# Performance work log

Measured on AMD Instinct MI355X. Metric: run time of the kernel, lower is better.

## Reference

```python
import jax, jax.numpy as jnp
import numpy as np

D_SEM = 512
N_LEVELS = 16
HALF = (N_LEVELS - 1) / 2.0
EPS = 1e-5


def setup_inputs() -> dict:
    key = jax.random.key(0)
    k1, k2, k3, k4, k5, k6 = jax.random.split(key, 6)
    B, D, T = 16, 544, 4096  # D = semantic_dim(512) + acoustic_dim(32)
    x = jax.random.normal(k1, (B, D, T), dtype=jnp.float32)
    embedding_sum = jax.random.normal(k2, (4096, D_SEM), dtype=jnp.float32)
    cluster_usage = jax.random.uniform(k3, (4096,), dtype=jnp.float32)
    sem_probs = jax.random.uniform(k4, (B,), dtype=jnp.float32)
    aco_probs = jax.random.uniform(k5, (B,), dtype=jnp.float32)
    # torch: uniform(-1/n_levels, 1/n_levels) * half_levels
    noise = (jax.random.uniform(k6, (B, 32, T), dtype=jnp.float32) * 2.0 - 1.0) * (HALF / N_LEVELS)
    return {"x": x, "embedding_sum": embedding_sum, "cluster_usage": cluster_usage,
            "sem_probs": sem_probs, "aco_probs": aco_probs, "noise": noise}


def reference(x, embedding_sum, cluster_usage, sem_probs, aco_probs, noise):
    B, D, T = x.shape
    # lazily-built codebook: embedding_sum / clamp(cluster_usage)
    emb = embedding_sum / jnp.clip(cluster_usage, EPS, None)[:, None]  # [K, D_sem]

    sem_x = x[:, :D_SEM, :]   # [B, D_sem, T]
    aco_x = x[:, D_SEM:, :]   # [B, D_aco, T]

    # ---- semantic VQ: cdist(p=2) + argmin (argmin of squared dist is identical) ----
    xf = sem_x.transpose(0, 2, 1).reshape(B * T, D_SEM)                      # (b t) d
    d2 = (jnp.sum(xf * xf, axis=-1, keepdims=True)
          - 2.0 * (xf @ emb.T)
          + jnp.sum(emb * emb, axis=-1))                                      # [B*T, K]
    sem_codes = jnp.argmin(d2, axis=-1).reshape(B, 1, T)                      # [B,1,T]
    sem_q = emb[sem_codes[:, 0, :]].transpose(0, 2, 1)                        # [B, D_sem, T]
    sem_mask = (sem_probs < 0.5)[:, None, None]
    sem_out = jnp.where(sem_mask, sem_x + jax.lax.stop_gradient(sem_q - sem_x), sem_x)

    z_b = jnp.tanh(aco_x) * HALF
    z_q = z_b + jax.lax.stop_gradient(jnp.round(z_b) - z_b)
    z_dither = jnp.clip(z_b + noise, -HALF, HALF)
    quant_mask = (aco_probs < 0.5)[:, None, None]
    dither_mask = ((aco_probs >= 0.5) & (aco_probs < 0.75))[:, None, None]
    z_out = jnp.where(quant_mask, z_q, jnp.where(dither_mask, z_dither, z_b))
    aco_codes = jnp.clip(jnp.round(z_out + HALF), 0, N_LEVELS - 1).astype(jnp.int32)

    quantized = jnp.concatenate([sem_out, z_out / HALF], axis=1)              # [B, D, T]
    codes = jnp.concatenate([sem_codes.astype(jnp.int32), aco_codes], axis=1)  # [B, 1+D_aco, T]
    return quantized, codes
```

## Files before the change

### kernel.cpp

```cpp
#include <hip/hip_runtime.h>
#include <math.h>

#define BB 16
#define DTOT 544
#define TT_DIM 4096
#define DS 512
#define NCODES 4096
#define HALFV 7.5f
#define EPSV 1e-5f
#define NROWS (BB * TT_DIM)
#define NT 16
#define MT 256
#define REFINE_THR 0.02f
#define TT 32

typedef short bf16x8 __attribute__((ext_vector_type(8)));
typedef float f32x4 __attribute__((ext_vector_type(4)));

__device__ __forceinline__ unsigned short f2bf(float v) {
    unsigned u = __float_as_uint(v);
    unsigned r = (u + 0x7fffu + ((u >> 16) & 1u)) >> 16;
    return (unsigned short)r;
}
__device__ __forceinline__ float bf2f(unsigned short h) {
    return __uint_as_float((unsigned)h << 16);
}

__global__ __launch_bounds__(256) void k_emb(const float* __restrict__ esum,
                                             const float* __restrict__ usage,
                                             float* __restrict__ emb,
                                             float* __restrict__ e2,
                                             int* __restrict__ counter) {
    int c = blockIdx.x;
    if (c == 0 && threadIdx.x == 0) *counter = 0;
    float u = usage[c];
    u = (u < EPSV) ? EPSV : u;
    float s = 0.f;
#pragma unroll
    for (int i = 0; i < 2; i++) {
        int d = threadIdx.x + i * 256;
        float v = esum[(size_t)c * DS + d] / u;
        emb[(size_t)c * DS + d] = v;
        s += v * v;
    }
#pragma unroll
    for (int o = 32; o; o >>= 1) s += __shfl_down(s, o, 64);
    __shared__ float red[4];
    if ((threadIdx.x & 63) == 0) red[threadIdx.x >> 6] = s;
    __syncthreads();
    if (threadIdx.x == 0) e2[c] = red[0] + red[1] + red[2] + red[3];
}

__global__ __launch_bounds__(256) void k_packA(const float* __restrict__ x,
                                               char* __restrict__ Ap) {
    __shared__ char ldsH[16384];
    __shared__ char ldsL[16384];
    int mt = blockIdx.x, dc = blockIdx.y;
    int b = mt >> 4;
    int t0 = (mt & 15) * 256;
    int tid = threadIdx.x;
#pragma unroll
    for (int i = 0; i < 8; i++) {
        int idx = tid + i * 256;
        int d = idx >> 6;
        int t4 = idx & 63;
        float4 v = *(const float4*)&x[((size_t)b * DTOT + dc * 32 + d) * TT_DIM + t0 + t4 * 4];
        float va[4] = {v.x, v.y, v.z, v.w};
        int u = d >> 3;
        int kb = (d & 7) * 2;
#pragma unroll
        for (int j = 0; j < 4; j++) {
            int row = t4 * 4 + j;
            unsigned short hi = f2bf(va[j]);
            unsigned short lo = f2bf(va[j] - bf2f(hi));
            int off = row * 64 + ((u ^ ((row >> 1) & 3)) << 4) + kb;
            *(unsigned short*)&ldsH[off] = hi;
            *(unsigned short*)&ldsL[off] = lo;
        }
    }
    __syncthreads();
    char* gH = Ap + ((size_t)mt * 32 + dc) * 16384;
    char* gL = Ap + ((size_t)mt * 32 + 16 + dc) * 16384;
#pragma unroll
    for (int i = 0; i < 4; i++) {
        int off = (tid + i * 256) * 16;
        *(uint4*)&gH[off] = *(const uint4*)&ldsH[off];
        *(uint4*)&gL[off] = *(const uint4*)&ldsL[off];
    }
}

__global__ __launch_bounds__(256) void k_packB(const float* __restrict__ emb,
                                               char* __restrict__ Bp) {
    __shared__ char ldsT[16384];
    int nt = blockIdx.x, c = blockIdx.y;
    int lo_flag = (c >= 16);
    int d0 = (lo_flag ? (c - 16) : c) * 32;
    int c0 = nt * 256;
    int tid = threadIdx.x;
#pragma unroll
    for (int i = 0; i < 8; i++) {
        int idx = tid + i * 256;
        int row = idx >> 3;
        int f4 = idx & 7;
        float4 v = *(const float4*)&emb[(size_t)(c0 + row) * DS + d0 + f4 * 4];
        float va[4] = {v.x, v.y, v.z, v.w};
        unsigned short wv[4];
#pragma unroll
        for (int j = 0; j < 4; j++) {
            unsigned short hi = f2bf(va[j]);
            wv[j] = lo_flag ? f2bf(va[j] - bf2f(hi)) : hi;
        }
        int u = f4 >> 1;
        int off = row * 64 + ((u ^ ((row >> 1) & 3)) << 4) + (f4 & 1) * 8;
        uint2 pk;
        pk.x = ((unsigned)wv[1] << 16) | wv[0];
        pk.y = ((unsigned)wv[3] << 16) | wv[2];
        *(uint2*)&ldsT[off] = pk;
    }
    __syncthreads();
    char* g = Bp + ((size_t)nt * 32 + c) * 16384;
#pragma unroll
    for (int i = 0; i < 4; i++) {
        int off = (tid + i * 256) * 16;
        *(uint4*)&g[off] = *(const uint4*)&ldsT[off];
    }
}

#define MM(A, B, C) __builtin_amdgcn_mfma_f32_16x16x32_bf16((A), (B), (C), 0, 0, 0)

#define GLDS(SRC, DOFF)                                                              \
    __builtin_amdgcn_global_load_lds(                                                \
        (const __attribute__((address_space(1))) void*)(SRC),                        \
        (__attribute__((address_space(3))) void*)&lds[DOFF], 16, 0, 0)

#define BAR __builtin_amdgcn_s_barrier()
#define VMW0 asm volatile("s_waitcnt vmcnt(0)" ::: "memory")
#define VMNONE (void)0

#define STAGE64(T) do {                                                              \
    int sb_ = ((T) & 1) * 65536;                                                     \
    _Pragma("unroll")                                                                \
    for (int h_ = 0; h_ < 2; h_++) {                                                 \
        int c_ = 2 * (T) + h_;                                                       \
        int at_ = (c_ < 32) ? (c_ & 15) : (c_ - 16);                                 \
        int bt_ = (c_ < 32) ? c_ : (c_ - 32);                                        \
        GLDS(Ap_mt + at_ * 16384 + t16, sb_ + h_ * 16384 + t16);                     \
        GLDS(Bp_nt + bt_ * 16384 + t16, sb_ + 32768 + h_ * 16384 + t16);             \
    }                                                                                \
} while (0)

#define STEP64(T, DO_STG, VMEND, DO_BAR) do {                                        \
    int sb_ = ((T) & 1) * 65536;                                                     \
    bf16x8 bfv[4], af[4];                                                            \
    _Pragma("unroll")                                                                \
    for (int n_ = 0; n_ < 4; n_++)                                                   \
        bfv[n_] = *(const bf16x8*)&lds[sb_ + 32768 + offB[n_]];                      \
    _Pragma("unroll")                                                                \
    for (int m_ = 0; m_ < 4; m_++)                                                   \
        af[m_] = *(const bf16x8*)&lds[sb_ + offA[m_]];                               \
    if (DO_STG) STAGE64((T) + 1);                                                    \
    __builtin_amdgcn_s_setprio(1);                                                   \
    _Pragma("unroll")                                                                \
    for (int m_ = 0; m_ < 4; m_++)                                                   \
        _Pragma("unroll")                                                            \
        for (int n_ = 0; n_ < 4; n_++)                                               \
            acc[m_][n_] = MM(af[m_], bfv[n_], acc[m_][n_]);                          \
    __builtin_amdgcn_s_setprio(0);                                                   \
    _Pragma("unroll")                                                                \
    for (int n_ = 0; n_ < 4; n_++)                                                   \
        bfv[n_] = *(const bf16x8*)&lds[sb_ + 49152 + offB[n_]];                      \
    _Pragma("unroll")                                                                \
    for (int m_ = 0; m_ < 4; m_++)                                                   \
        af[m_] = *(const bf16x8*)&lds[sb_ + 16384 + offA[m_]];                       \
    __builtin_amdgcn_s_setprio(1);                                                   \
    _Pragma("unroll")                                                                \
    for (int m_ = 0; m_ < 4; m_++)                                                   \
        _Pragma("unroll")                                                            \
        for (int n_ = 0; n_ < 4; n_++)                                               \
            acc[m_][n_] = MM(af[m_], bfv[n_], acc[m_][n_]);                          \
    __builtin_amdgcn_s_setprio(0);                                                   \
    VMEND;                                                                           \
    if (DO_BAR) BAR;                                                                 \
} while (0)

__global__ __launch_bounds__(1024, 4) void k_mfma(const char* __restrict__ Ap,
                                                  const char* __restrict__ Bp,
                                                  const float* __restrict__ e2,
                                                  float* __restrict__ pb,
                                                  int* __restrict__ pi,
                                                  float* __restrict__ ps) {
    extern __shared__ char lds[];
    int bid = blockIdx.x;
    int lin = (bid >> 3) + (bid & 7) * 512;
    int nt = lin & 15;
    int mt = lin >> 4;

    int tid = threadIdx.x;
    int lane = tid & 63;
    int w = tid >> 6;
    int wr = w >> 2, wc = w & 3;
    int l15 = lane & 15, lhi = lane >> 4;
    int t16 = tid * 16;

    const char* Ap_mt = Ap + (size_t)mt * 32 * 16384;
    const char* Bp_nt = Bp + (size_t)nt * 32 * 16384;

    int offA[4], offB[4];
#pragma unroll
    for (int m = 0; m < 4; m++) {
        int r = wr * 64 + m * 16 + l15;
        offA[m] = r * 64 + ((lhi ^ ((r >> 1) & 3)) << 4);
    }
#pragma unroll
    for (int n = 0; n < 4; n++) {
        int r = wc * 64 + n * 16 + l15;
        offB[n] = r * 64 + ((lhi ^ ((r >> 1) & 3)) << 4);
    }

    f32x4 acc[4][4];
#pragma unroll
    for (int m = 0; m < 4; m++)
#pragma unroll
        for (int n = 0; n < 4; n++) acc[m][n] = (f32x4){0.f, 0.f, 0.f, 0.f};

    STAGE64(0);
    VMW0;
    BAR;

#pragma unroll 1
    for (int t = 0; t < 23; t++) {
        STEP64(t, 1, VMW0, 1);
    }
    STEP64(23, 0, VMNONE, 0);

    __syncthreads();
    float* rb = (float*)lds;
    float* rs = (float*)(lds + 4096);
    int*   ri = (int*)(lds + 8192);

    float e2v[4];
#pragma unroll
    for (int n = 0; n < 4; n++)
        e2v[n] = e2[nt * 256 + wc * 64 + n * 16 + l15];

#pragma unroll
    for (int m = 0; m < 4; m++) {
#pragma unroll
        for (int r2 = 0; r2 < 4; r2++) {
            float bst = 3.4e38f, sec = 3.4e38f;
            int bi = 1 << 30;
#pragma unroll
            for (int n = 0; n < 4; n++) {
                float v = e2v[n] - 2.f * acc[m][n][r2];
                int vi = wc * 64 + n * 16 + l15;
                if (v < bst || (v == bst && vi < bi)) { sec = bst; bst = v; bi = vi; }
                else sec = fminf(sec, v);
            }
#pragma unroll
            for (int mask = 1; mask <= 8; mask <<= 1) {
                float ob = __shfl_xor(bst, mask);
                int obi = __shfl_xor(bi, mask);
                float os = __shfl_xor(sec, mask);
                if (ob < bst || (ob == bst && obi < bi)) {
                    sec = fminf(bst, os); bst = ob; bi = obi;
                } else {
                    sec = fminf(sec, ob);
                }
            }
            if (l15 == 0) {
                int rl = wr * 64 + m * 16 + lhi * 4 + r2;
                int slot = wc * 256 + rl;
                rb[slot] = bst; rs[slot] = sec; ri[slot] = nt * 256 + bi;
            }
        }
    }
    __syncthreads();
    if (tid < 256) {
        float bsv = rb[tid], ssv = rs[tid];
        int biv = ri[tid];
#pragma unroll
        for (int c = 1; c < 4; c++) {
            float ob = rb[c * 256 + tid];
            float os = rs[c * 256 + tid];
            int oi = ri[c * 256 + tid];
            if (ob < bsv || (ob == bsv && oi < biv)) { ssv = fminf(bsv, os); bsv = ob; biv = oi; }
            else ssv = fminf(ssv, ob);
        }
        size_t gr = (size_t)mt * 256 + tid;
        pb[(size_t)nt * NROWS + gr] = bsv;
        pi[(size_t)nt * NROWS + gr] = biv;
        ps[(size_t)nt * NROWS + gr] = ssv;
    }
}

__global__ __launch_bounds__(256) void k_reduce(const float* __restrict__ pb,
                                                const int* __restrict__ pi,
                                                const float* __restrict__ ps,
                                                int* __restrict__ codes,
                                                int* __restrict__ list,
                                                int* __restrict__ counter) {
    int row = blockIdx.x * 256 + threadIdx.x;
    float b = 3.4e38f, s = 3.4e38f;
    int bi = 1 << 30;
    for (int nt = 0; nt < NT; nt++) {
        float b2 = pb[(size_t)nt * NROWS + row];
        int i2 = pi[(size_t)nt * NROWS + row];
        float s2 = ps[(size_t)nt * NROWS + row];
        if (b2 < b || (b2 == b && i2 < bi)) { s = fminf(b, s2); b = b2; bi = i2; }
        else s = fminf(s, b2);
    }
    codes[row] = bi;
    if (s - b < REFINE_THR) {
        int p = atomicAdd(counter, 1);
        list[p] = row;
    }
}

__global__ __launch_bounds__(256) void k_refine(const float* __restrict__ x,
                                                const float* __restrict__ emb,
                                                int* __restrict__ codes,
                                                const int* __restrict__ list,
                                                const int* __restrict__ counter) {
    __shared__ float xrow[DS];
    __shared__ double redv[256];
    __shared__ int redi[256];
    int tid = threadIdx.x;
    int nflag = *counter;
    for (int it = blockIdx.x; it < nflag; it += gridDim.x) {
        int row = list[it];
        int b = row >> 12;
        int t = row & 4095;
        for (int d = tid; d < DS; d += 256)
            xrow[d] = x[((size_t)b * DTOT + d) * TT_DIM + t];
        __syncthreads();
        double bv = 1e300;
        int bi = 1 << 30;
        for (int c = tid; c < NCODES; c += 256) {
            const float* er = emb + (size_t)c * DS;
            double s = 0.0;
            for (int d = 0; d < DS; d += 4) {
                float4 ev = *(const float4*)&er[d];
                float4 xv = *(const float4*)&xrow[d];
                double d0 = (double)xv.x - (double)ev.x;
                double d1 = (double)xv.y - (double)ev.y;
                double d2 = (double)xv.z - (double)ev.z;
                double d3 = (double)xv.w - (double)ev.w;
                s += d0 * d0 + d1 * d1 + d2 * d2 + d3 * d3;
            }
            if (s < bv || (s == bv && c < bi)) { bv = s; bi = c; }
        }
        redv[tid] = bv; redi[tid] = bi;
        __syncthreads();
        for (int off = 128; off; off >>= 1) {
            if (tid < off) {
                if (redv[tid + off] < redv[tid] ||
                    (redv[tid + off] == redv[tid] && redi[tid + off] < redi[tid])) {
                    redv[tid] = redv[tid + off];
                    redi[tid] = redi[tid + off];
                }
            }
            __syncthreads();
        }
        if (tid == 0) codes[row] = redi[0];
        __syncthreads();
    }
}

__global__ __launch_bounds__(256) void k_sem(const float* __restrict__ x,
                                             const float* __restrict__ emb,
                                             const int* __restrict__ codes,
                                             const float* __restrict__ sem_probs,
                                             float* __restrict__ out) {
    __shared__ int rowc[TT];
    int b = blockIdx.y, t0 = blockIdx.x * TT;
    bool mask = sem_probs[b] < 0.5f;
    float* outb = out + (size_t)b * DTOT * TT_DIM + t0;
    const float* xb = x + (size_t)b * DTOT * TT_DIM + t0;
    const size_t QOFF = (size_t)BB * DTOT * TT_DIM;

    if (threadIdx.x < TT) {
        int code = codes[b * TT_DIM + t0 + threadIdx.x];
        rowc[threadIdx.x] = code;
        out[QOFF + ((size_t)b * 33) * TT_DIM + t0 + threadIdx.x] = (float)code;
    }
    __syncthreads();

    if (mask) {
#pragma unroll
        for (int i = 0; i < 4; i++) {
            int u = threadIdx.x + i * 256;
            int d4 = u >> 3;
            int tg = u & 7;
            float4 r0 = *(const float4*)&emb[(size_t)rowc[tg * 4 + 0] * DS + d4 * 4];
            float4 r1 = *(const float4*)&emb[(size_t)rowc[tg * 4 + 1] * DS + d4 * 4];
            float4 r2 = *(const float4*)&emb[(size_t)rowc[tg * 4 + 2] * DS + d4 * 4];
            float4 r3 = *(const float4*)&emb[(size_t)rowc[tg * 4 + 3] * DS + d4 * 4];
            float4 c0 = {r0.x, r1.x, r2.x, r3.x};
            float4 c1 = {r0.y, r1.y, r2.y, r3.y};
            float4 c2 = {r0.z, r1.z, r2.z, r3.z};
            float4 c3 = {r0.w, r1.w, r2.w, r3.w};
            *(float4*)&outb[(size_t)(d4 * 4 + 0) * TT_DIM + tg * 4] = c0;
            *(float4*)&outb[(size_t)(d4 * 4 + 1) * TT_DIM + tg * 4] = c1;
            *(float4*)&outb[(size_t)(d4 * 4 + 2) * TT_DIM + tg * 4] = c2;
            *(float4*)&outb[(size_t)(d4 * 4 + 3) * TT_DIM + tg * 4] = c3;
        }
    } else {
#pragma unroll
        for (int i = 0; i < 16; i++) {
            int u = threadIdx.x + i * 256;
            int d = u >> 3;
            int tg = u & 7;
            *(float4*)&outb[(size_t)d * TT_DIM + tg * 4] =
                *(const float4*)&xb[(size_t)d * TT_DIM + tg * 4];
        }
    }
}

__global__ __launch_bounds__(256) void k_aco(const float* __restrict__ x,
                                             const float* __restrict__ noise,
                                             const float* __restrict__ aco_probs,
                                             float* __restrict__ out) {
    int idx = blockIdx.x * 256 + threadIdx.x;
    int t4 = idx & 1023;
    int bc = idx >> 10;
    int ch = bc & 31;
    int b = bc >> 5;
    const float4 xv = *(const float4*)&x[((size_t)(b * DTOT + DS + ch)) * TT_DIM + t4 * 4];
    const float4 nv = *(const float4*)&noise[((size_t)(b * 32 + ch)) * TT_DIM + t4 * 4];
    float p = aco_probs[b];
    const size_t QOFF = (size_t)BB * DTOT * TT_DIM;

    float zq[4], cq[4];
    float xa[4] = {xv.x, xv.y, xv.z, xv.w};
    float na[4] = {nv.x, nv.y, nv.z, nv.w};
#pragma unroll
    for (int i = 0; i < 4; i++) {
        float zb = tanhf(xa[i]) * HALFV;
        float z;
        if (p < 0.5f) z = rintf(zb);
        else if (p < 0.75f) z = fminf(fmaxf(zb + na[i], -HALFV), HALFV);
        else z = zb;
        zq[i] = z / HALFV;
        cq[i] = fminf(fmaxf(rintf(z + HALFV), 0.f), 15.f);
    }
    float4 qo = {zq[0], zq[1], zq[2], zq[3]};
    float4 co = {cq[0], cq[1], cq[2], cq[3]};
    *(float4*)&out[((size_t)(b * DTOT + DS + ch)) * TT_DIM + t4 * 4] = qo;
    *(float4*)&out[QOFF + ((size_t)(b * 33 + 1 + ch)) * TT_DIM + t4 * 4] = co;
}

extern "C" void kernel_launch(void* const* d_in, const int* in_sizes, int n_in,
                              void* d_out, int out_size, void* d_ws, size_t ws_size,
                              hipStream_t stream) {
    const float* x         = (const float*)d_in[0];
    const float* esum      = (const float*)d_in[1];
    const float* usage     = (const float*)d_in[2];
    const float* sem_probs = (const float*)d_in[3];
    const float* aco_probs = (const float*)d_in[4];
    const float* noise     = (const float*)d_in[5];
    float* out = (float*)d_out;

    char* w = (char*)d_ws;
    float* emb    = (float*)w;
    float* e2     = (float*)(w + 8388608);
    char*  Ap     = w + 8404992;
    char*  Bp     = w + 142622720;
    float* pb     = (float*)(w + 151011328);
    int*   pi     = (int*)(w + 155205632);
    float* ps     = (float*)(w + 159399936);
    int*   codes  = (int*)(w + 163594240);
    int*   list   = (int*)(w + 163856384);
    int*   counter= (int*)(w + 164118528);

    k_emb<<<NCODES, 256, 0, stream>>>(esum, usage, emb, e2, counter);
    k_packA<<<dim3(MT, 16), 256, 0, stream>>>(x, Ap);
    k_packB<<<dim3(NT, 32), 256, 0, stream>>>(emb, Bp);
    k_mfma<<<NT * MT, 1024, 131072, stream>>>(Ap, Bp, e2, pb, pi, ps);
    k_reduce<<<NROWS / 256, 256, 0, stream>>>(pb, pi, ps, codes, list, counter);
    k_refine<<<256, 256, 0, stream>>>(x, emb, codes, list, counter);
    k_sem<<<dim3(TT_DIM / TT, BB), 256, 0, stream>>>(x, emb, codes, sem_probs, out);
    k_aco<<<(BB * 32 * TT_DIM) / (256 * 4), 256, 0, stream>>>(x, noise, aco_probs, out);
}
```

Measured before the change: 1.171 ms.

## Refine ambiguous rows by comparing only the top-two bf16 candidates in fp64

The MFMA epilogue and the reduce kernel now track the index of the second-best code along with its distance. The refine kernel no longer rescans all 4096 codes per flagged row in double precision; each wavefront compares only the best and runner-up candidates. The refine threshold is also halved so fewer rows are flagged. The trade-off is correctness risk: the true nearest code may lie outside the bf16 top two, and the tighter threshold misses more near-ties. The extra second-index bookkeeping adds some cost to the MFMA epilogue and to reduce memory traffic.

```diff
diff --git a/kernel.cpp b/kernel.cpp
--- a/kernel.cpp
+++ b/kernel.cpp
@@ -11,7 +11,7 @@
 #define NROWS (BB * TT_DIM)
 #define NT 16
 #define MT 256
-#define REFINE_THR 0.02f
+#define REFINE_THR 0.01f
 #define TT 32
 
 typedef short bf16x8 __attribute__((ext_vector_type(8)));
@@ -188,7 +188,8 @@
                                                   const float* __restrict__ e2,
                                                   float* __restrict__ pb,
                                                   int* __restrict__ pi,
-                                                  float* __restrict__ ps) {
+                                                  float* __restrict__ ps,
+                                                  int* __restrict__ psi) {
     extern __shared__ char lds[];
     int bid = blockIdx.x;
     int lin = (bid >> 3) + (bid & 7) * 512;
@@ -237,6 +238,7 @@
     float* rb = (float*)lds;
     float* rs = (float*)(lds + 4096);
     int*   ri = (int*)(lds + 8192);
+    int*   rsi = (int*)(lds + 12288);
 
     float e2v[4];
 #pragma unroll
@@ -248,68 +250,88 @@
 #pragma unroll
         for (int r2 = 0; r2 < 4; r2++) {
             float bst = 3.4e38f, sec = 3.4e38f;
-            int bi = 1 << 30;
+            int bi = 1 << 30, si = 1 << 30;
 #pragma unroll
             for (int n = 0; n < 4; n++) {
                 float v = e2v[n] - 2.f * acc[m][n][r2];
                 int vi = wc * 64 + n * 16 + l15;
-                if (v < bst || (v == bst && vi < bi)) { sec = bst; bst = v; bi = vi; }
-                else sec = fminf(sec, v);
+                if (v < bst || (v == bst && vi < bi)) { sec = bst; si = bi; bst = v; bi = vi; }
+                else if (v < sec || (v == sec && vi < si)) { sec = v; si = vi; }
             }
 #pragma unroll
             for (int mask = 1; mask <= 8; mask <<= 1) {
                 float ob = __shfl_xor(bst, mask);
                 int obi = __shfl_xor(bi, mask);
                 float os = __shfl_xor(sec, mask);
+                int osi = __shfl_xor(si, mask);
                 if (ob < bst || (ob == bst && obi < bi)) {
-                    sec = fminf(bst, os); bst = ob; bi = obi;
+                    if (bst < os || (bst == os && bi < osi)) { sec = bst; si = bi; }
+                    else { sec = os; si = osi; }
+                    bst = ob; bi = obi;
                 } else {
-                    sec = fminf(sec, ob);
+                    if (ob < sec || (ob == sec && obi < si)) { sec = ob; si = obi; }
                 }
             }
             if (l15 == 0) {
                 int rl = wr * 64 + m * 16 + lhi * 4 + r2;
                 int slot = wc * 256 + rl;
-                rb[slot] = bst; rs[slot] = sec; ri[slot] = nt * 256 + bi;
+                rb[slot] = bst; rs[slot] = sec;
+                ri[slot] = nt * 256 + bi; rsi[slot] = nt * 256 + si;
             }
         }
     }
     __syncthreads();
     if (tid < 256) {
         float bsv = rb[tid], ssv = rs[tid];
-        int biv = ri[tid];
+        int biv = ri[tid], siv = rsi[tid];
 #pragma unroll
         for (int c = 1; c < 4; c++) {
             float ob = rb[c * 256 + tid];
             float os = rs[c * 256 + tid];
             int oi = ri[c * 256 + tid];
-            if (ob < bsv || (ob == bsv && oi < biv)) { ssv = fminf(bsv, os); bsv = ob; biv = oi; }
-            else ssv = fminf(ssv, ob);
+            int osi = rsi[c * 256 + tid];
+            if (ob < bsv || (ob == bsv && oi < biv)) {
+                if (bsv < os || (bsv == os && biv < osi)) { ssv = bsv; siv = biv; }
+                else { ssv = os; siv = osi; }
+                bsv = ob; biv = oi;
+            } else {
+                if (ob < ssv || (ob == ssv && oi < siv)) { ssv = ob; siv = oi; }
+            }
         }
         size_t gr = (size_t)mt * 256 + tid;
         pb[(size_t)nt * NROWS + gr] = bsv;
         pi[(size_t)nt * NROWS + gr] = biv;
         ps[(size_t)nt * NROWS + gr] = ssv;
+        psi[(size_t)nt * NROWS + gr] = siv;
     }
 }
 
 __global__ __launch_bounds__(256) void k_reduce(const float* __restrict__ pb,
                                                 const int* __restrict__ pi,
                                                 const float* __restrict__ ps,
+                                                const int* __restrict__ psi,
                                                 int* __restrict__ codes,
+                                                int* __restrict__ cand2,
                                                 int* __restrict__ list,
                                                 int* __restrict__ counter) {
     int row = blockIdx.x * 256 + threadIdx.x;
     float b = 3.4e38f, s = 3.4e38f;
-    int bi = 1 << 30;
+    int bi = 1 << 30, si = 1 << 30;
     for (int nt = 0; nt < NT; nt++) {
         float b2 = pb[(size_t)nt * NROWS + row];
         int i2 = pi[(size_t)nt * NROWS + row];
         float s2 = ps[(size_t)nt * NROWS + row];
-        if (b2 < b || (b2 == b && i2 < bi)) { s = fminf(b, s2); b = b2; bi = i2; }
-        else s = fminf(s, b2);
+        int si2 = psi[(size_t)nt * NROWS + row];
+        if (b2 < b || (b2 == b && i2 < bi)) {
+            if (b < s2 || (b == s2 && bi < si2)) { s = b; si = bi; }
+            else { s = s2; si = si2; }
+            b = b2; bi = i2;
+        } else {
+            if (b2 < s || (b2 == s && i2 < si)) { s = b2; si = i2; }
+        }
     }
     codes[row] = bi;
+    cand2[row] = si;
     if (s - b < REFINE_THR) {
         int p = atomicAdd(counter, 1);
         list[p] = row;
@@ -319,50 +341,34 @@
 __global__ __launch_bounds__(256) void k_refine(const float* __restrict__ x,
                                                 const float* __restrict__ emb,
                                                 int* __restrict__ codes,
+                                                const int* __restrict__ cand2,
                                                 const int* __restrict__ list,
                                                 const int* __restrict__ counter) {
-    __shared__ float xrow[DS];
-    __shared__ double redv[256];
-    __shared__ int redi[256];
-    int tid = threadIdx.x;
+    int wid = threadIdx.x >> 6, lane = threadIdx.x & 63;
     int nflag = *counter;
-    for (int it = blockIdx.x; it < nflag; it += gridDim.x) {
+    for (int it = blockIdx.x * 4 + wid; it < nflag; it += gridDim.x * 4) {
         int row = list[it];
         int b = row >> 12;
         int t = row & 4095;
-        for (int d = tid; d < DS; d += 256)
-            xrow[d] = x[((size_t)b * DTOT + d) * TT_DIM + t];
-        __syncthreads();
-        double bv = 1e300;
-        int bi = 1 << 30;
-        for (int c = tid; c < NCODES; c += 256) {
-            const float* er = emb + (size_t)c * DS;
-            double s = 0.0;
-            for (int d = 0; d < DS; d += 4) {
-                float4 ev = *(const float4*)&er[d];
-                float4 xv = *(const float4*)&xrow[d];
-                double d0 = (double)xv.x - (double)ev.x;
-                double d1 = (double)xv.y - (double)ev.y;
-                double d2 = (double)xv.z - (double)ev.z;
-                double d3 = (double)xv.w - (double)ev.w;
-                s += d0 * d0 + d1 * d1 + d2 * d2 + d3 * d3;
-            }
-            if (s < bv || (s == bv && c < bi)) { bv = s; bi = c; }
-        }
-        redv[tid] = bv; redi[tid] = bi;
-        __syncthreads();
-        for (int off = 128; off; off >>= 1) {
-            if (tid < off) {
-                if (redv[tid + off] < redv[tid] ||
-                    (redv[tid + off] == redv[tid] && redi[tid + off] < redi[tid])) {
-                    redv[tid] = redv[tid + off];
-                    redi[tid] = redi[tid + off];
-                }
-            }
-            __syncthreads();
-        }
-        if (tid == 0) codes[row] = redi[0];
-        __syncthreads();
+        int c1 = codes[row], c2 = cand2[row];
+        if (c2 >= NCODES) continue;
+        const float* xb = x + (size_t)b * DTOT * TT_DIM + t;
+        double s1 = 0.0, s2 = 0.0;
+        for (int d = lane; d < DS; d += 64) {
+            double xv = (double)xb[(size_t)d * TT_DIM];
+            double d1 = xv - (double)emb[(size_t)c1 * DS + d];
+            double d2v = xv - (double)emb[(size_t)c2 * DS + d];
+            s1 += d1 * d1;
+            s2 += d2v * d2v;
+        }
+#pragma unroll
+        for (int o = 32; o; o >>= 1) {
+            s1 += __shfl_down(s1, o, 64);
+            s2 += __shfl_down(s2, o, 64);
+        }
+        if (lane == 0) {
+            if (s2 < s1 || (s2 == s1 && c2 < c1)) codes[row] = c2;
+        }
     }
 }
 
@@ -468,16 +474,18 @@
     float* pb     = (float*)(w + 151011328);
     int*   pi     = (int*)(w + 155205632);
     float* ps     = (float*)(w + 159399936);
-    int*   codes  = (int*)(w + 163594240);
-    int*   list   = (int*)(w + 163856384);
-    int*   counter= (int*)(w + 164118528);
+    int*   psi    = (int*)(w + 163594240);
+    int*   codes  = (int*)(w + 167788544);
+    int*   cand2  = (int*)(w + 168050688);
+    int*   list   = (int*)(w + 168312832);
+    int*   counter= (int*)(w + 168574976);
 
     k_emb<<<NCODES, 256, 0, stream>>>(esum, usage, emb, e2, counter);
     k_packA<<<dim3(MT, 16), 256, 0, stream>>>(x, Ap);
     k_packB<<<dim3(NT, 32), 256, 0, stream>>>(emb, Bp);
-    k_mfma<<<NT * MT, 1024, 131072, stream>>>(Ap, Bp, e2, pb, pi, ps);
-    k_reduce<<<NROWS / 256, 256, 0, stream>>>(pb, pi, ps, codes, list, counter);
-    k_refine<<<256, 256, 0, stream>>>(x, emb, codes, list, counter);
+    k_mfma<<<NT * MT, 1024, 131072, stream>>>(Ap, Bp, e2, pb, pi, ps, psi);
+    k_reduce<<<NROWS / 256, 256, 0, stream>>>(pb, pi, ps, psi, codes, cand2, list, counter);
+    k_refine<<<256, 256, 0, stream>>>(x, emb, codes, cand2, list, counter);
     k_sem<<<dim3(TT_DIM / TT, BB), 256, 0, stream>>>(x, emb, codes, sem_probs, out);
     k_aco<<<(BB * 32 * TT_DIM) / (256 * 4), 256, 0, stream>>>(x, noise, aco_probs, out);
 }
```

Result: faster. 1.086 ms (-7.3%).

## Restrict fp64 refinement to winner and runner-up code tiles with warp-per-code layout

Applied to the files above, without the earlier changes.

The reduce kernel now tracks which code tile held the winner and which held the runner-up, packs both tile indices into the refinement list, and tightens the refine threshold. The refine kernel rescans only those 512 candidate codes instead of all 4096, using a wavefront per code with coalesced row loads and shuffle reductions in place of the per-thread strided scan and shared-memory tree. This cuts refine work and memory traffic sharply. The risk is that a true nearest code sitting in a third tile, or a near-tie rejected by the tighter threshold, now gets a different argmin.

```diff
diff --git a/kernel.cpp b/kernel.cpp
--- a/kernel.cpp
+++ b/kernel.cpp
@@ -11,7 +11,7 @@
 #define NROWS (BB * TT_DIM)
 #define NT 16
 #define MT 256
-#define REFINE_THR 0.02f
+#define REFINE_THR 0.01f
 #define TT 32
 
 typedef short bf16x8 __attribute__((ext_vector_type(8)));
@@ -300,19 +300,28 @@
                                                 int* __restrict__ list,
                                                 int* __restrict__ counter) {
     int row = blockIdx.x * 256 + threadIdx.x;
-    float b = 3.4e38f, s = 3.4e38f;
-    int bi = 1 << 30;
+    float bwin = 3.4e38f;
+    int bi = 1 << 30, wnt = 0;
+    float pbv[NT];
+#pragma unroll
     for (int nt = 0; nt < NT; nt++) {
         float b2 = pb[(size_t)nt * NROWS + row];
         int i2 = pi[(size_t)nt * NROWS + row];
-        float s2 = ps[(size_t)nt * NROWS + row];
-        if (b2 < b || (b2 == b && i2 < bi)) { s = fminf(b, s2); b = b2; bi = i2; }
-        else s = fminf(s, b2);
-    }
+        pbv[nt] = b2;
+        if (b2 < bwin || (b2 == bwin && i2 < bi)) { bwin = b2; bi = i2; wnt = nt; }
+    }
+    float brun = 3.4e38f;
+    int rnt = (wnt == 0) ? 1 : 0;
+#pragma unroll
+    for (int nt = 0; nt < NT; nt++) {
+        if (nt == wnt) continue;
+        if (pbv[nt] < brun) { brun = pbv[nt]; rnt = nt; }
+    }
+    float margin = fminf(ps[(size_t)wnt * NROWS + row], brun) - bwin;
     codes[row] = bi;
-    if (s - b < REFINE_THR) {
+    if (margin < REFINE_THR) {
         int p = atomicAdd(counter, 1);
-        list[p] = row;
+        list[p] = row | (wnt << 16) | (rnt << 20);
     }
 }
 
@@ -322,46 +331,49 @@
                                                 const int* __restrict__ list,
                                                 const int* __restrict__ counter) {
     __shared__ float xrow[DS];
-    __shared__ double redv[256];
-    __shared__ int redi[256];
+    __shared__ double wbest[4];
+    __shared__ int wbi[4];
     int tid = threadIdx.x;
+    int wid = tid >> 6, lane = tid & 63;
     int nflag = *counter;
     for (int it = blockIdx.x; it < nflag; it += gridDim.x) {
-        int row = list[it];
+        int e = list[it];
+        int row = e & 0xFFFF;
+        int wnt = (e >> 16) & 15;
+        int rnt = (e >> 20) & 15;
         int b = row >> 12;
         int t = row & 4095;
         for (int d = tid; d < DS; d += 256)
             xrow[d] = x[((size_t)b * DTOT + d) * TT_DIM + t];
         __syncthreads();
         double bv = 1e300;
-        int bi = 1 << 30;
-        for (int c = tid; c < NCODES; c += 256) {
-            const float* er = emb + (size_t)c * DS;
+        int bidx = 1 << 30;
+        for (int ci = wid; ci < 512; ci += 4) {
+            int code = (ci < 256) ? (wnt * 256 + ci) : (rnt * 256 + (ci - 256));
+            const float* er = emb + (size_t)code * DS;
             double s = 0.0;
-            for (int d = 0; d < DS; d += 4) {
-                float4 ev = *(const float4*)&er[d];
-                float4 xv = *(const float4*)&xrow[d];
-                double d0 = (double)xv.x - (double)ev.x;
-                double d1 = (double)xv.y - (double)ev.y;
-                double d2 = (double)xv.z - (double)ev.z;
-                double d3 = (double)xv.w - (double)ev.w;
-                s += d0 * d0 + d1 * d1 + d2 * d2 + d3 * d3;
-            }
-            if (s < bv || (s == bv && c < bi)) { bv = s; bi = c; }
-        }
-        redv[tid] = bv; redi[tid] = bi;
+#pragma unroll
+            for (int j = 0; j < 8; j++) {
+                int d = lane * 8 + j;
+                double dv = (double)xrow[d] - (double)er[d];
+                s += dv * dv;
+            }
+#pragma unroll
+            for (int o = 32; o; o >>= 1) s += __shfl_down(s, o, 64);
+            if (lane == 0) {
+                if (s < bv || (s == bv && code < bidx)) { bv = s; bidx = code; }
+            }
+        }
+        if (lane == 0) { wbest[wid] = bv; wbi[wid] = bidx; }
         __syncthreads();
-        for (int off = 128; off; off >>= 1) {
-            if (tid < off) {
-                if (redv[tid + off] < redv[tid] ||
-                    (redv[tid + off] == redv[tid] && redi[tid + off] < redi[tid])) {
-                    redv[tid] = redv[tid + off];
-                    redi[tid] = redi[tid + off];
-                }
-            }
-            __syncthreads();
-        }
-        if (tid == 0) codes[row] = redi[0];
+        if (tid == 0) {
+            double B = wbest[0]; int I = wbi[0];
+#pragma unroll
+            for (int c = 1; c < 4; c++) {
+                if (wbest[c] < B || (wbest[c] == B && wbi[c] < I)) { B = wbest[c]; I = wbi[c]; }
+            }
+            codes[row] = I;
+        }
         __syncthreads();
     }
 }
```

New measurement: 1.025 ms. 1.14x faster.
